# Performance work log

Measured on AMD Instinct MI355X. Metric: run time of the kernel, lower is better.

The kernel has to match this reference:

```python
import jax, jax.numpy as jnp
import numpy as np

N_EMBD = 1024
N_HEAD = 16
HEAD_DIM = N_EMBD // N_HEAD  # 64
LATENT_DIM = N_EMBD // 2     # 512
B, T = 4, 2048


def setup_inputs() -> dict:
    key = jax.random.key(0)
    ks = jax.random.split(key, 5)
    # weights stored [in, out] so forward is x @ W (equivalent to torch Linear with W.T)
    def init(k, fan_in, fan_out):
        bound = 1.0 / np.sqrt(fan_in)
        return jax.random.uniform(k, (fan_in, fan_out), jnp.float32, -bound, bound)
    return {
        "x": jax.random.normal(ks[0], (B, T, N_EMBD), jnp.float32),
        "Wc_down": init(ks[1], N_EMBD, LATENT_DIM),
        "Wq_up": init(ks[2], LATENT_DIM, N_EMBD),
        "Wkv_up": init(ks[3], LATENT_DIM, 2 * HEAD_DIM),
        "Wc_proj": init(ks[4], N_EMBD, N_EMBD),
    }


def reference(x, Wc_down, Wq_up, Wkv_up, Wc_proj):
    Bsz, Tlen, C = x.shape
    latent = x @ Wc_down                                    # [B,T,latent]
    q = (latent @ Wq_up).reshape(Bsz, Tlen, N_HEAD, HEAD_DIM)  # [B,T,H,D]
    kv = latent @ Wkv_up                                    # [B,T,2D]
    k, v = kv[..., :HEAD_DIM], kv[..., HEAD_DIM:]           # shared across heads (MQA)
    scale = 1.0 / np.sqrt(HEAD_DIM)
    att = jnp.einsum("bthd,bsd->bhts", q, k) * scale        # [B,H,T,T]
    causal = jnp.tril(jnp.ones((Tlen, Tlen), dtype=bool))
    att = jnp.where(causal[None, None], att, -jnp.inf)
    att = jax.nn.softmax(att, axis=-1)
    y = jnp.einsum("bhts,bsd->bthd", att, v).reshape(Bsz, Tlen, C)
    return y @ Wc_proj
```

## Files before the change

kernel.cpp:

```cpp
#include <hip/hip_runtime.h>
#include <hip/hip_bf16.h>


typedef __attribute__((ext_vector_type(8))) short bf16x8;
typedef __attribute__((ext_vector_type(4))) float floatx4;

#define B_   4
#define T_   2048
#define C_   1024
#define H_   16
#define D_   64
#define L_   512
#define QKV_N 1152

__device__ __forceinline__ float EXP2F(float x) {
    float r;
    asm("v_exp_f32 %0, %1" : "=v"(r) : "v"(x));
    return r;
}

__device__ __forceinline__ unsigned short f2bf(float f) {
    unsigned int x = __float_as_uint(f);
    unsigned int r = (x + 0x7fffu + ((x >> 16) & 1u)) >> 16;
    return (unsigned short)r;
}

__device__ __forceinline__ unsigned int cvtpk_bf(float lo, float hi) {
    unsigned int r;
    asm("v_cvt_pk_bf16_f32 %0, %1, %2" : "=v"(r) : "v"(lo), "v"(hi));
    return r;
}

__device__ __forceinline__ void gload_lds16(const unsigned short* g, char* l) {
    __builtin_amdgcn_global_load_lds(
        (const __attribute__((address_space(1))) void*)g,
        (__attribute__((address_space(3))) void*)l,
        16, 0, 0);
}

__global__ void cvt_bf16(const float* __restrict__ X, unsigned short* __restrict__ Xb, int n4) {
    int i = blockIdx.x * 256 + threadIdx.x;
    if (i >= n4) return;
    float4 v = *(const float4*)(X + (size_t)i * 4);
    ushort4 o;
    o.x = f2bf(v.x); o.y = f2bf(v.y); o.z = f2bf(v.z); o.w = f2bf(v.w);
    *(ushort4*)(Xb + (size_t)i * 4) = o;
}

__global__ void wtrans(const float* __restrict__ W, unsigned short* __restrict__ Wt,
                       int K, int N, float scale) {
    int idx = blockIdx.x * 256 + threadIdx.x;
    if (idx >= K * N) return;
    int n = idx / K, k = idx - n * K;
    Wt[idx] = f2bf(W[(size_t)k * N + n] * scale);
}

__global__ void vtrans(const unsigned short* __restrict__ qkv, unsigned short* __restrict__ Vt) {
    int idx = blockIdx.x * 256 + threadIdx.x;
    int t = idx & (T_ - 1);
    int d = (idx >> 11) & 63;
    int b = idx >> 17;
    Vt[idx] = qkv[((size_t)(b * T_ + t)) * QKV_N + 1024 + 64 + d];
}

#define BM 128
#define BN 128
#define BK 64

template <bool F32OUT>
__global__ __launch_bounds__(256) void gemm_bt(const unsigned short* __restrict__ A,
                                               const unsigned short* __restrict__ Bt,
                                               void* __restrict__ Cout,
                                               int M, int N, int K) {
    __shared__ __align__(16) char ldsA[BM * BK * 2];
    __shared__ __align__(16) char ldsB[BN * BK * 2];
    const int tid = threadIdx.x;
    const int lane = tid & 63, wave = tid >> 6;
    const int lrow = lane & 15, lhi = lane >> 4;
    const int bm = blockIdx.y * BM, bn = blockIdx.x * BN;
    const int wm = (wave >> 1) * 64, wn = (wave & 1) * 64;

    floatx4 acc[4][4] = {};

    for (int k0 = 0; k0 < K; k0 += BK) {
#pragma unroll
        for (int i = 0; i < 4; ++i) {
            int c = tid + i * 256;
            int row = c >> 3;
            int sc = ((c & 7) ^ (row & 7)) * 8;
            gload_lds16(A + (size_t)(bm + row) * K + k0 + sc,
                        ldsA + (i * 256 + wave * 64) * 16);
            gload_lds16(Bt + (size_t)(bn + row) * K + k0 + sc,
                        ldsB + (i * 256 + wave * 64) * 16);
        }
        __syncthreads();
#pragma unroll
        for (int kk = 0; kk < 2; ++kk) {
            bf16x8 af[4], bfr[4];
#pragma unroll
            for (int m = 0; m < 4; ++m) {
                int row = wm + m * 16 + lrow;
                int colb = kk * 64 + lhi * 16;
                af[m] = *(const bf16x8*)(ldsA + row * 128 + (colb ^ ((row & 7) << 4)));
            }
#pragma unroll
            for (int n = 0; n < 4; ++n) {
                int row = wn + n * 16 + lrow;
                int colb = kk * 64 + lhi * 16;
                bfr[n] = *(const bf16x8*)(ldsB + row * 128 + (colb ^ ((row & 7) << 4)));
            }
#pragma unroll
            for (int m = 0; m < 4; ++m)
#pragma unroll
                for (int n = 0; n < 4; ++n)
                    acc[m][n] = __builtin_amdgcn_mfma_f32_16x16x32_bf16(af[m], bfr[n], acc[m][n], 0, 0, 0);
        }
        __syncthreads();
    }
#pragma unroll
    for (int m = 0; m < 4; ++m)
#pragma unroll
        for (int n = 0; n < 4; ++n)
#pragma unroll
            for (int r = 0; r < 4; ++r) {
                int row = bm + wm + m * 16 + lhi * 4 + r;
                int col = bn + wn + n * 16 + lrow;
                float v = acc[m][n][r];
                if (F32OUT)
                    ((float*)Cout)[(size_t)row * N + col] = v;
                else
                    ((unsigned short*)Cout)[(size_t)row * N + col] = f2bf(v);
            }
}

__global__ __launch_bounds__(256) void flash(const unsigned short* __restrict__ QKV,
                                             const unsigned short* __restrict__ Vt,
                                             unsigned short* __restrict__ Y) {
    const int id = blockIdx.x;
    const int qt = 15 - (id >> 6);
    const int h = (id >> 2) & 15;
    const int b = id & 3;
    const int tid = threadIdx.x;
    const int lane = tid & 63, wave = tid >> 6;
    const int lrow = lane & 15, lhi = lane >> 4;

    __shared__ __align__(16) char ldsK[2][64 * 128];
    __shared__ __align__(16) char ldsV[2][64 * 128];
    __shared__ __align__(16) char ldsP[4][32 * 128];

    const int qbase = qt * 128 + wave * 32;
    const unsigned short* KV = QKV + 1024;
    const int nst = qt * 2 + 2;

    const unsigned short* kvp[2];
    const unsigned short* vtp[2];
#pragma unroll
    for (int i = 0; i < 2; ++i) {
        int c = tid + i * 256;
        int row = c >> 3;
        int sc = ((c & 7) ^ (row & 7)) * 8;
        kvp[i] = KV + ((size_t)(b * T_ + row)) * QKV_N + sc;
        vtp[i] = Vt + ((size_t)(b * 64 + row)) * T_ + sc;
    }

    bf16x8 qf[2][2];
#pragma unroll
    for (int nf = 0; nf < 2; ++nf)
#pragma unroll
        for (int kk = 0; kk < 2; ++kk) {
            int trow = b * T_ + qbase + nf * 16 + lrow;
            int col = h * 64 + kk * 32 + lhi * 8;
            qf[nf][kk] = *(const bf16x8*)(QKV + (size_t)trow * QKV_N + col);
        }

    floatx4 o[2][4] = {};
    floatx4 ol[2] = {};

    const short one_bf = (short)0x3F80;
    const bf16x8 ones8 = {one_bf, one_bf, one_bf, one_bf, one_bf, one_bf, one_bf, one_bf};

#pragma unroll
    for (int i = 0; i < 2; ++i) {
        gload_lds16(kvp[i], ldsK[0] + (i * 256 + wave * 64) * 16);
        gload_lds16(vtp[i], ldsV[0] + (i * 256 + wave * 64) * 16);
        kvp[i] += 64 * QKV_N;
        vtp[i] += 64;
    }
    __syncthreads();

    auto dostep = [&](int st, int buf) __attribute__((always_inline)) {
        char* kbuf = ldsK[buf];
        char* vbuf = ldsV[buf];
        char* nkbuf = ldsK[buf ^ 1];
        char* nvbuf = ldsV[buf ^ 1];
        if (st + 1 < nst) {
#pragma unroll
            for (int i = 0; i < 2; ++i) {
                gload_lds16(kvp[i], nkbuf + (i * 256 + wave * 64) * 16);
                gload_lds16(vtp[i], nvbuf + (i * 256 + wave * 64) * 16);
                kvp[i] += 64 * QKV_N;
                vtp[i] += 64;
            }
        }

        if (st * 64 <= qbase + 31) {
            floatx4 s[4][2] = {};
#pragma unroll
            for (int kk = 0; kk < 2; ++kk) {
                bf16x8 kf[4];
#pragma unroll
                for (int mf = 0; mf < 4; ++mf) {
                    int row = mf * 16 + lrow;
                    int colb = kk * 64 + lhi * 16;
                    kf[mf] = *(const bf16x8*)(kbuf + row * 128 + (colb ^ ((row & 7) << 4)));
                }
#pragma unroll
                for (int mf = 0; mf < 4; ++mf)
#pragma unroll
                    for (int nf = 0; nf < 2; ++nf)
                        s[mf][nf] = __builtin_amdgcn_mfma_f32_16x16x32_bf16(kf[mf], qf[nf][kk], s[mf][nf], 0, 0, 0);
            }

#pragma unroll
            for (int nf = 0; nf < 2; ++nf) {
                if (st * 64 + 63 > qbase + nf * 16) {
                    int qg = qbase + nf * 16 + lrow;
#pragma unroll
                    for (int mf = 0; mf < 4; ++mf)
#pragma unroll
                        for (int r = 0; r < 4; ++r) {
                            int sg = st * 64 + mf * 16 + lhi * 4 + r;
                            if (sg > qg) s[mf][nf][r] = -1e30f;
                        }
                }
#pragma unroll
                for (int mf = 0; mf < 4; ++mf)
#pragma unroll
                    for (int rr = 0; rr < 4; ++rr)
                        s[mf][nf][rr] = EXP2F(s[mf][nf][rr]);
            }

#pragma unroll
            for (int mf = 0; mf < 4; ++mf)
#pragma unroll
                for (int nf = 0; nf < 2; ++nf) {
                    uint2 pk;
                    pk.x = cvtpk_bf(s[mf][nf][0], s[mf][nf][1]);
                    pk.y = cvtpk_bf(s[mf][nf][2], s[mf][nf][3]);
                    int row = nf * 16 + lrow;
                    int colb = (mf * 16 + lhi * 4) * 2;
                    *(uint2*)(ldsP[wave] + row * 128 + (colb ^ ((row & 7) << 4))) = pk;
                }

#pragma unroll
            for (int ss = 0; ss < 2; ++ss) {
                bf16x8 pf[2], vf[4];
#pragma unroll
                for (int m = 0; m < 2; ++m) {
                    int row = m * 16 + lrow;
                    int colb = ss * 64 + lhi * 16;
                    pf[m] = *(const bf16x8*)(ldsP[wave] + row * 128 + (colb ^ ((row & 7) << 4)));
                }
#pragma unroll
                for (int dn = 0; dn < 4; ++dn) {
                    int row = dn * 16 + lrow;
                    int colb = ss * 64 + lhi * 16;
                    vf[dn] = *(const bf16x8*)(vbuf + row * 128 + (colb ^ ((row & 7) << 4)));
                }
#pragma unroll
                for (int m = 0; m < 2; ++m) {
#pragma unroll
                    for (int dn = 0; dn < 4; ++dn)
                        o[m][dn] = __builtin_amdgcn_mfma_f32_16x16x32_bf16(pf[m], vf[dn], o[m][dn], 0, 0, 0);
                    ol[m] = __builtin_amdgcn_mfma_f32_16x16x32_bf16(pf[m], ones8, ol[m], 0, 0, 0);
                }
            }
        }
        __syncthreads();
    };

    for (int st = 0; st < nst; st += 2) {
        dostep(st, 0);
        dostep(st + 1, 1);
    }

#pragma unroll
    for (int m = 0; m < 2; ++m) {
        float linv[4];
#pragma unroll
        for (int rr = 0; rr < 4; ++rr) linv[rr] = __builtin_amdgcn_rcpf(ol[m][rr]);
#pragma unroll
        for (int dn = 0; dn < 4; ++dn)
#pragma unroll
            for (int rr = 0; rr < 4; ++rr) {
                int trow = b * T_ + qbase + m * 16 + lhi * 4 + rr;
                int col = h * 64 + dn * 16 + lrow;
                Y[(size_t)trow * C_ + col] = f2bf(o[m][dn][rr] * linv[rr]);
            }
    }
}

extern "C" void kernel_launch(void* const* d_in, const int* in_sizes, int n_in,
                              void* d_out, int out_size, void* d_ws, size_t ws_size,
                              hipStream_t stream) {
    (void)in_sizes; (void)n_in; (void)out_size; (void)ws_size;
    const float* x   = (const float*)d_in[0];
    const float* Wd  = (const float*)d_in[1];
    const float* Wq  = (const float*)d_in[2];
    const float* Wkv = (const float*)d_in[3];
    const float* Wp  = (const float*)d_in[4];
    float* out = (float*)d_out;
    char* ws = (char*)d_ws;

    const int BT = B_ * T_;
    const float KSC = 0.125f * 1.44269504f;

    unsigned short* xb     = (unsigned short*)(ws + 0);
    unsigned short* wdT    = (unsigned short*)(ws + 16777216);
    unsigned short* wqkvT  = (unsigned short*)(ws + 17825792);
    unsigned short* wpT    = (unsigned short*)(ws + 19005440);
    unsigned short* latent = (unsigned short*)(ws + 21102592);
    unsigned short* qkv    = (unsigned short*)(ws + 29491200);
    unsigned short* vt     = (unsigned short*)(ws + 48365568);
    unsigned short* yb     = xb;

    cvt_bf16<<<(BT * C_ / 4 + 255) / 256, 256, 0, stream>>>(x, xb, BT * C_ / 4);
    wtrans<<<(C_ * L_ + 255) / 256, 256, 0, stream>>>(Wd, wdT, C_, L_, 1.0f);
    wtrans<<<(L_ * C_ + 255) / 256, 256, 0, stream>>>(Wq, wqkvT, L_, C_, KSC);
    wtrans<<<(L_ * 128 + 255) / 256, 256, 0, stream>>>(Wkv, wqkvT + 1024 * 512, L_, 128, 1.0f);
    wtrans<<<(C_ * C_ + 255) / 256, 256, 0, stream>>>(Wp, wpT, C_, C_, 1.0f);

    gemm_bt<false><<<dim3(L_ / BN, BT / BM), 256, 0, stream>>>(xb, wdT, latent, BT, L_, C_);
    gemm_bt<false><<<dim3(QKV_N / BN, BT / BM), 256, 0, stream>>>(latent, wqkvT, qkv, BT, QKV_N, L_);

    vtrans<<<(B_ * 64 * T_ + 255) / 256, 256, 0, stream>>>(qkv, vt);

    flash<<<1024, 256, 0, stream>>>(qkv, vt, yb);

    gemm_bt<true><<<dim3(C_ / BN, BT / BM), 256, 0, stream>>>(yb, wpT, out, BT, C_, C_);
}
```

Measured before the change: 156.3 us.

## Enlarge flash query tile and switch to triple-buffered K/V pipeline

Each flash block now covers 256 query rows (64 per wave) rather than 128, halving the grid and doubling the reuse of each loaded K/V tile. K/V staging moves from a double buffer with a full __syncthreads per step to a rotating triple buffer, using a partial vmcnt wait plus a single barrier. MFMA sections are wrapped in setprio and launch bounds request two blocks per CU. The cost is higher register and LDS use: P scratch doubles to 64 rows and the accumulators double. The last iteration issues a redundant reload so the vmcnt accounting stays uniform.

```diff
diff --git a/kernel.cpp b/kernel.cpp
--- a/kernel.cpp
+++ b/kernel.cpp
@@ -133,39 +133,39 @@
             }
 }
 
-__global__ __launch_bounds__(256) void flash(const unsigned short* __restrict__ QKV,
-                                             const unsigned short* __restrict__ Vt,
-                                             unsigned short* __restrict__ Y) {
+__global__ __launch_bounds__(256, 2) void flash(const unsigned short* __restrict__ QKV,
+                                                const unsigned short* __restrict__ Vt,
+                                                unsigned short* __restrict__ Y) {
     const int id = blockIdx.x;
-    const int qt = 15 - (id >> 6);
+    const int qt = 7 - (id >> 6);
     const int h = (id >> 2) & 15;
     const int b = id & 3;
     const int tid = threadIdx.x;
     const int lane = tid & 63, wave = tid >> 6;
     const int lrow = lane & 15, lhi = lane >> 4;
 
-    __shared__ __align__(16) char ldsK[2][64 * 128];
-    __shared__ __align__(16) char ldsV[2][64 * 128];
-    __shared__ __align__(16) char ldsP[4][32 * 128];
-
-    const int qbase = qt * 128 + wave * 32;
+    __shared__ __align__(16) char ldsK[3][64 * 128];
+    __shared__ __align__(16) char ldsV[3][64 * 128];
+    __shared__ __align__(16) char ldsP[4][64 * 128];
+
+    const int qbase = qt * 256 + wave * 64;
     const unsigned short* KV = QKV + 1024;
-    const int nst = qt * 2 + 2;
-
-    const unsigned short* kvp[2];
-    const unsigned short* vtp[2];
+    const int nst = qt * 4 + 4;
+
+    const unsigned short* kp[2];
+    const unsigned short* vp[2];
 #pragma unroll
     for (int i = 0; i < 2; ++i) {
         int c = tid + i * 256;
         int row = c >> 3;
         int sc = ((c & 7) ^ (row & 7)) * 8;
-        kvp[i] = KV + ((size_t)(b * T_ + row)) * QKV_N + sc;
-        vtp[i] = Vt + ((size_t)(b * 64 + row)) * T_ + sc;
-    }
-
-    bf16x8 qf[2][2];
-#pragma unroll
-    for (int nf = 0; nf < 2; ++nf)
+        kp[i] = KV + ((size_t)(b * T_ + row)) * QKV_N + sc;
+        vp[i] = Vt + ((size_t)(b * 64 + row)) * T_ + sc;
+    }
+
+    bf16x8 qf[4][2];
+#pragma unroll
+    for (int nf = 0; nf < 4; ++nf)
 #pragma unroll
         for (int kk = 0; kk < 2; ++kk) {
             int trow = b * T_ + qbase + nf * 16 + lrow;
@@ -173,38 +173,41 @@
             qf[nf][kk] = *(const bf16x8*)(QKV + (size_t)trow * QKV_N + col);
         }
 
-    floatx4 o[2][4] = {};
-    floatx4 ol[2] = {};
+    floatx4 o[4][4] = {};
+    floatx4 ol[4] = {};
 
     const short one_bf = (short)0x3F80;
     const bf16x8 ones8 = {one_bf, one_bf, one_bf, one_bf, one_bf, one_bf, one_bf, one_bf};
 
+    char* kcur = ldsK[0];  char* kstg = ldsK[1];  char* kfre = ldsK[2];
+    char* vcur = ldsV[0];  char* vstg = ldsV[1];  char* vfre = ldsV[2];
 #pragma unroll
     for (int i = 0; i < 2; ++i) {
-        gload_lds16(kvp[i], ldsK[0] + (i * 256 + wave * 64) * 16);
-        gload_lds16(vtp[i], ldsV[0] + (i * 256 + wave * 64) * 16);
-        kvp[i] += 64 * QKV_N;
-        vtp[i] += 64;
-    }
-    __syncthreads();
-
-    auto dostep = [&](int st, int buf) __attribute__((always_inline)) {
-        char* kbuf = ldsK[buf];
-        char* vbuf = ldsV[buf];
-        char* nkbuf = ldsK[buf ^ 1];
-        char* nvbuf = ldsV[buf ^ 1];
-        if (st + 1 < nst) {
-#pragma unroll
-            for (int i = 0; i < 2; ++i) {
-                gload_lds16(kvp[i], nkbuf + (i * 256 + wave * 64) * 16);
-                gload_lds16(vtp[i], nvbuf + (i * 256 + wave * 64) * 16);
-                kvp[i] += 64 * QKV_N;
-                vtp[i] += 64;
-            }
-        }
-
-        if (st * 64 <= qbase + 31) {
-            floatx4 s[4][2] = {};
+        gload_lds16(kp[i], kcur + (i * 256 + wave * 64) * 16);
+        gload_lds16(vp[i], vcur + (i * 256 + wave * 64) * 16);
+        kp[i] += 64 * QKV_N;
+        vp[i] += 64;
+    }
+
+    for (int st = 0; st < nst; ++st) {
+        const bool more = (st + 1 < nst);
+        const long kadj = more ? 0 : -(long)(64 * QKV_N);
+        const long vadj = more ? 0 : -64L;
+#pragma unroll
+        for (int i = 0; i < 2; ++i) {
+            gload_lds16(kp[i] + kadj, kstg + (i * 256 + wave * 64) * 16);
+            gload_lds16(vp[i] + vadj, vstg + (i * 256 + wave * 64) * 16);
+        }
+        if (more) {
+            kp[0] += 64 * QKV_N; kp[1] += 64 * QKV_N;
+            vp[0] += 64;         vp[1] += 64;
+        }
+        asm volatile("s_waitcnt vmcnt(4)" ::: "memory");
+        __builtin_amdgcn_s_barrier();
+        __builtin_amdgcn_sched_barrier(0);
+
+        if (st * 64 <= qbase + 63) {
+            floatx4 s[4][4] = {};
 #pragma unroll
             for (int kk = 0; kk < 2; ++kk) {
                 bf16x8 kf[4];
@@ -212,17 +215,19 @@
                 for (int mf = 0; mf < 4; ++mf) {
                     int row = mf * 16 + lrow;
                     int colb = kk * 64 + lhi * 16;
-                    kf[mf] = *(const bf16x8*)(kbuf + row * 128 + (colb ^ ((row & 7) << 4)));
-                }
+                    kf[mf] = *(const bf16x8*)(kcur + row * 128 + (colb ^ ((row & 7) << 4)));
+                }
+                __builtin_amdgcn_s_setprio(1);
 #pragma unroll
                 for (int mf = 0; mf < 4; ++mf)
 #pragma unroll
-                    for (int nf = 0; nf < 2; ++nf)
+                    for (int nf = 0; nf < 4; ++nf)
                         s[mf][nf] = __builtin_amdgcn_mfma_f32_16x16x32_bf16(kf[mf], qf[nf][kk], s[mf][nf], 0, 0, 0);
-            }
-
-#pragma unroll
-            for (int nf = 0; nf < 2; ++nf) {
+                __builtin_amdgcn_s_setprio(0);
+            }
+
+#pragma unroll
+            for (int nf = 0; nf < 4; ++nf) {
                 if (st * 64 + 63 > qbase + nf * 16) {
                     int qg = qbase + nf * 16 + lrow;
 #pragma unroll
@@ -243,7 +248,7 @@
 #pragma unroll
             for (int mf = 0; mf < 4; ++mf)
 #pragma unroll
-                for (int nf = 0; nf < 2; ++nf) {
+                for (int nf = 0; nf < 4; ++nf) {
                     uint2 pk;
                     pk.x = cvtpk_bf(s[mf][nf][0], s[mf][nf][1]);
                     pk.y = cvtpk_bf(s[mf][nf][2], s[mf][nf][3]);
@@ -254,9 +259,9 @@
 
 #pragma unroll
             for (int ss = 0; ss < 2; ++ss) {
-                bf16x8 pf[2], vf[4];
-#pragma unroll
-                for (int m = 0; m < 2; ++m) {
+                bf16x8 pf[4], vf[4];
+#pragma unroll
+                for (int m = 0; m < 4; ++m) {
                     int row = m * 16 + lrow;
                     int colb = ss * 64 + lhi * 16;
                     pf[m] = *(const bf16x8*)(ldsP[wave] + row * 128 + (colb ^ ((row & 7) << 4)));
@@ -265,27 +270,27 @@
                 for (int dn = 0; dn < 4; ++dn) {
                     int row = dn * 16 + lrow;
                     int colb = ss * 64 + lhi * 16;
-                    vf[dn] = *(const bf16x8*)(vbuf + row * 128 + (colb ^ ((row & 7) << 4)));
-                }
-#pragma unroll
-                for (int m = 0; m < 2; ++m) {
+                    vf[dn] = *(const bf16x8*)(vcur + row * 128 + (colb ^ ((row & 7) << 4)));
+                }
+                __builtin_amdgcn_s_setprio(1);
+#pragma unroll
+                for (int m = 0; m < 4; ++m) {
 #pragma unroll
                     for (int dn = 0; dn < 4; ++dn)
                         o[m][dn] = __builtin_amdgcn_mfma_f32_16x16x32_bf16(pf[m], vf[dn], o[m][dn], 0, 0, 0);
                     ol[m] = __builtin_amdgcn_mfma_f32_16x16x32_bf16(pf[m], ones8, ol[m], 0, 0, 0);
                 }
-            }
-        }
-        __syncthreads();
-    };
-
-    for (int st = 0; st < nst; st += 2) {
-        dostep(st, 0);
-        dostep(st + 1, 1);
-    }
-
-#pragma unroll
-    for (int m = 0; m < 2; ++m) {
+                __builtin_amdgcn_s_setprio(0);
+            }
+        }
+
+        char* t;
+        t = kcur; kcur = kstg; kstg = kfre; kfre = t;
+        t = vcur; vcur = vstg; vstg = vfre; vfre = t;
+    }
+
+#pragma unroll
+    for (int m = 0; m < 4; ++m) {
         float linv[4];
 #pragma unroll
         for (int rr = 0; rr < 4; ++rr) linv[rr] = __builtin_amdgcn_rcpf(ol[m][rr]);
@@ -335,7 +340,7 @@
 
     vtrans<<<(B_ * 64 * T_ + 255) / 256, 256, 0, stream>>>(qkv, vt);
 
-    flash<<<1024, 256, 0, stream>>>(qkv, vt, yb);
+    flash<<<512, 256, 0, stream>>>(qkv, vt, yb);
 
     gemm_bt<true><<<dim3(C_ / BN, BT / BM), 256, 0, stream>>>(yb, wpT, out, BT, C_, C_);
 }
```

New measurement: 156.5 us. Within noise of the previous version (+0.1%).
